# Kernel tuning notes

Hardware: AMD Instinct MI355X
Metric: run time of the kernel (lower is better)

The kernel has to match this reference:

```python
import jax, jax.numpy as jnp
import numpy as np

NUM_EXPERTS = 8
TOP_K = 2
N_TOKENS = 4096
HIDDEN = 1024
EXPERT_DIM = 4096


def setup_inputs() -> dict:
    key = jax.random.key(0)
    ks = jax.random.split(key, 4)
    x = jax.random.normal(ks[0], (N_TOKENS, HIDDEN), dtype=jnp.float32)
    Wg = jax.random.normal(ks[1], (HIDDEN, NUM_EXPERTS), dtype=jnp.float32) * 0.02
    bg = jnp.zeros((NUM_EXPERTS,), dtype=jnp.float32)
    W1 = jax.random.normal(ks[2], (NUM_EXPERTS, HIDDEN, EXPERT_DIM), dtype=jnp.float32) * 0.02
    b1 = jnp.zeros((NUM_EXPERTS, EXPERT_DIM), dtype=jnp.float32)
    W2 = jax.random.normal(ks[3], (NUM_EXPERTS, EXPERT_DIM, HIDDEN), dtype=jnp.float32) * 0.02
    b2 = jnp.zeros((NUM_EXPERTS, HIDDEN), dtype=jnp.float32)
    return {"x": x, "Wg": Wg, "bg": bg, "W1": W1, "b1": b1, "W2": W2, "b2": b2}


def reference(x, Wg, bg, W1, b1, W2, b2):
    # Gating: softmax over experts, then top-k routing with renormalized gates.
    gate_probs = jax.nn.softmax(x @ Wg + bg, axis=-1)          # [N, E]
    top_gates, top_idx = jax.lax.top_k(gate_probs, TOP_K)      # [N, K]
    top_gates = top_gates / jnp.sum(top_gates, axis=-1, keepdims=True)
    # Per-(token, expert) combine weight: sum of gates routed to that expert.
    combine = jnp.sum(
        jax.nn.one_hot(top_idx, NUM_EXPERTS, dtype=x.dtype) * top_gates[..., None],
        axis=1,
    )  # [N, E]
    # Expert MLPs: Linear -> ReLU -> Linear (dropout=0 at eval, norm=False).
    out = jnp.zeros_like(x)
    for e in range(NUM_EXPERTS):
        h = jax.nn.relu(x @ W1[e] + b1[e])                      # [N, expert_dim]
        y = h @ W2[e] + b2[e]                                   # [N, hidden]
        out = out + combine[:, e:e + 1] * y
    # Switch-style auxiliary load-balancing loss.
    expert_counts = jnp.sum(gate_probs, axis=0)                 # [E]
    expert_fractions = expert_counts / jnp.sum(expert_counts)
    gate_means = jnp.mean(gate_probs, axis=0)
    aux_loss = NUM_EXPERTS * jnp.sum(expert_fractions * gate_means)
    return out, aux_loss
```

## Files before the change

### kernel.cpp

```cpp
#include <hip/hip_runtime.h>


typedef unsigned short u16;
typedef __bf16 bf16x8 __attribute__((ext_vector_type(8)));
typedef float  f32x4  __attribute__((ext_vector_type(4)));

#define NTOK 4096
#define HID  1024
#define EDIM 4096
#define NEXP 8
#define MAXMT 40

__device__ __forceinline__ u16 f32_bf16(float f) {
  unsigned int u = __float_as_uint(f);
  u += 0x7FFFu + ((u >> 16) & 1u);
  return (u16)(u >> 16);
}

__global__ void gate_kernel(const float* __restrict__ x,
                            const float* __restrict__ Wg,
                            const float* __restrict__ bg,
                            float* __restrict__ combine,
                            float* __restrict__ counts,
                            int* __restrict__ icnt,
                            int* __restrict__ top2idx,
                            float* __restrict__ top2g) {
  __shared__ float lc[NEXP];
  int t = threadIdx.x;
  if (t < NEXP) lc[t] = 0.f;
  __syncthreads();
  int token = blockIdx.x * 4 + (t >> 6);
  int lane = t & 63;
  float s[NEXP] = {};
  const float* xr = x + (size_t)token * HID;
  for (int h = lane; h < HID; h += 64) {
    float xv = xr[h];
    const float* wrow = Wg + (size_t)h * NEXP;
#pragma unroll
    for (int e = 0; e < NEXP; ++e) s[e] += xv * wrow[e];
  }
#pragma unroll
  for (int off = 32; off > 0; off >>= 1) {
#pragma unroll
    for (int e = 0; e < NEXP; ++e) s[e] += __shfl_xor(s[e], off);
  }
  float m = -1e30f;
#pragma unroll
  for (int e = 0; e < NEXP; ++e) { s[e] += bg[e]; m = fmaxf(m, s[e]); }
  float p[NEXP]; float sum = 0.f;
#pragma unroll
  for (int e = 0; e < NEXP; ++e) { p[e] = expf(s[e] - m); sum += p[e]; }
  float inv = 1.f / sum;
#pragma unroll
  for (int e = 0; e < NEXP; ++e) p[e] *= inv;
  int i1 = 0; float g1 = p[0];
#pragma unroll
  for (int e = 1; e < NEXP; ++e) if (p[e] > g1) { g1 = p[e]; i1 = e; }
  int i2 = -1; float g2 = -1.f;
#pragma unroll
  for (int e = 0; e < NEXP; ++e) if (e != i1 && p[e] > g2) { g2 = p[e]; i2 = e; }
  float ginv = 1.f / (g1 + g2);
  if (lane == 0) {
#pragma unroll
    for (int e = 0; e < NEXP; ++e) {
      float c = (e == i1) ? g1 * ginv : (e == i2) ? g2 * ginv : 0.f;
      combine[(size_t)token * NEXP + e] = c;
      atomicAdd(&lc[e], p[e]);
    }
    top2idx[token * 2] = i1; top2idx[token * 2 + 1] = i2;
    top2g[token * 2] = g1 * ginv; top2g[token * 2 + 1] = g2 * ginv;
    atomicAdd(&icnt[i1], 1); atomicAdd(&icnt[i2], 1);
  }
  __syncthreads();
  if (t < NEXP) atomicAdd(&counts[t], lc[t]);
}

__global__ void aux_kernel(const float* __restrict__ counts, float* __restrict__ aux_out) {
  float s = 0.f;
#pragma unroll
  for (int e = 0; e < NEXP; ++e) s += counts[e];
  float a = 0.f;
#pragma unroll
  for (int e = 0; e < NEXP; ++e) a += (counts[e] / s) * (counts[e] / (float)NTOK);
  aux_out[0] = (float)NEXP * a;
}

__global__ void off_kernel(const int* __restrict__ icnt, int* __restrict__ ioff,
                           int* __restrict__ cursor, int* __restrict__ nmtP,
                           int* __restrict__ mtE, int* __restrict__ mtRow0,
                           int* __restrict__ mtValid) {
  int s = 0;
  int loc[NEXP];
  for (int e = 0; e < NEXP; ++e) { loc[e] = s; ioff[e] = s; s += icnt[e]; cursor[e] = 0; }
  int nm = 0;
  for (int e = 0; e < NEXP; ++e) {
    int c = icnt[e];
    int tiles = (c + 255) >> 8;
    for (int mt = 0; mt < tiles; ++mt) {
      mtE[nm] = e; mtRow0[nm] = loc[e] + (mt << 8);
      int v = c - (mt << 8); mtValid[nm] = v > 256 ? 256 : v;
      nm++;
    }
  }
  nmtP[0] = nm;
}

__global__ void fill_kernel(const int* __restrict__ top2idx, const int* __restrict__ ioff,
                            int* __restrict__ cursor, int* __restrict__ tok) {
  int i = blockIdx.x * 256 + threadIdx.x;
  if (i >= NTOK * 2) return;
  int t = i >> 1, k = i & 1;
  int e = top2idx[i];
  int pos = atomicAdd(&cursor[e], 1);
  tok[ioff[e] + pos] = t | (k << 16);
}

__global__ void cvt_kernel(const float* __restrict__ in, u16* __restrict__ out) {
  size_t i = ((size_t)blockIdx.x * 256 + threadIdx.x) * 4;
  float4 v = *(const float4*)(in + i);
  ushort4 o = make_ushort4(f32_bf16(v.x), f32_bf16(v.y), f32_bf16(v.z), f32_bf16(v.w));
  *(ushort4*)(out + i) = o;
}

__global__ __launch_bounds__(256) void cvtT_kernel(const float* __restrict__ W,
                                                   u16* __restrict__ WT, int R, int C) {
  __shared__ u16 tile[64][66];
  int t = threadIdx.x;
  size_t eoff = (size_t)blockIdx.z * R * C;
  int c0 = blockIdx.x * 64, r0 = blockIdx.y * 64;
  const float* Wp = W + eoff + (size_t)r0 * C + c0;
  u16* WTp = WT + eoff + (size_t)c0 * R + r0;
#pragma unroll
  for (int p = 0; p < 4; ++p) {
    int idx = p * 256 + t;
    int row = idx >> 4;
    int col = (idx & 15) * 4;
    float4 v = *(const float4*)(Wp + (size_t)row * C + col);
    tile[row][col + 0] = f32_bf16(v.x);
    tile[row][col + 1] = f32_bf16(v.y);
    tile[row][col + 2] = f32_bf16(v.z);
    tile[row][col + 3] = f32_bf16(v.w);
  }
  __syncthreads();
#pragma unroll
  for (int p = 0; p < 4; ++p) {
    int idx = p * 256 + t;
    int oc = idx >> 4;
    int orow = (idx & 15) * 4;
    ushort4 o;
    o.x = tile[orow + 0][oc];
    o.y = tile[orow + 1][oc];
    o.z = tile[orow + 2][oc];
    o.w = tile[orow + 3][oc];
    *(ushort4*)(WTp + (size_t)oc * R + orow) = o;
  }
}

template<int MODE, int SPLITK>
__global__ __launch_bounds__(256, 2) void gemm_sparse(
    const u16* __restrict__ A, const u16* __restrict__ Wt,
    const int* __restrict__ nmtP, const int* __restrict__ mtE,
    const int* __restrict__ mtRow0, const int* __restrict__ mtValid,
    const int* __restrict__ tok,
    const float* __restrict__ bias, u16* __restrict__ Hout,
    float* __restrict__ Y0, float* __restrict__ Y1)
{
  constexpr int KDIM = (MODE == 1) ? HID : EDIM;
  constexpr int NDIM = (MODE == 1) ? EDIM : HID;
  constexpr int NT = NDIM / 128;
  constexpr int NK = KDIM / 32 / SPLITK;

  const int nwg = gridDim.x;
  const int q = nwg >> 3, rr8 = nwg & 7;
  const int xcd = blockIdx.x & 7, jj = blockIdx.x >> 3;
  int item = (xcd < rr8 ? xcd * (q + 1) : rr8 * (q + 1) + (xcd - rr8) * q) + jj;

  if (item >= nmtP[0] * NT * SPLITK) return;
  const int gmt = item / (NT * SPLITK);
  const int sk  = (item / NT) % SPLITK;
  const int nt  = item % NT;
  const int e = mtE[gmt], row0 = mtRow0[gmt], valid = mtValid[gmt];
  const int kbeg = sk * (KDIM / SPLITK);

  __shared__ __align__(16) u16 As[3][256 * 32];
  __shared__ __align__(16) u16 Bs[3][128 * 32];
  const int t = threadIdx.x;
  const int lane = t & 63;
  const int w = t >> 6;
  const int wr = w >> 1, wc = w & 1;
  const int bn0 = nt << 7;
  const int kq = lane >> 4;
  const int r  = lane & 15;

  const u16* Bb = Wt + ((size_t)e * NDIM + bn0) * KDIM;

  size_t arow[4];
#pragma unroll
  for (int c = 0; c < 4; ++c) {
    int idx = c * 256 + t;
    int row = idx >> 2;
    if (MODE == 1) {
      int rw = (row < valid) ? row : 0;
      arow[c] = (size_t)(tok[row0 + rw] & 0xFFFF) * KDIM;
    } else {
      arow[c] = (size_t)(row0 + row) * KDIM;
    }
  }

  auto stage = [&](int buf, int k0) {
#pragma unroll
    for (int c = 0; c < 4; ++c) {
      int idx = c * 256 + t;
      int row = idx >> 2;
      int kc  = (((idx & 3) ^ ((row >> 1) & 3))) << 3;
      __builtin_amdgcn_global_load_lds(
          (const __attribute__((address_space(1))) void*)(A + arow[c] + k0 + kc),
          (__attribute__((address_space(3))) void*)(&As[buf][idx * 8]), 16, 0, 0);
    }
#pragma unroll
    for (int c = 0; c < 2; ++c) {
      int idx = c * 256 + t;
      int row = idx >> 2;
      int kc  = (((idx & 3) ^ ((row >> 1) & 3))) << 3;
      __builtin_amdgcn_global_load_lds(
          (const __attribute__((address_space(1))) void*)(Bb + (size_t)row * KDIM + k0 + kc),
          (__attribute__((address_space(3))) void*)(&Bs[buf][idx * 8]), 16, 0, 0);
    }
  };

  f32x4 acc[4][8] = {};

  stage(0, kbeg);
  stage(1, kbeg + 32);
  int cb = 0, sb = 2;
  for (int ks = 0; ks < NK; ++ks) {
    if (ks + 1 < NK) asm volatile("s_waitcnt vmcnt(6)" ::: "memory");
    else             asm volatile("s_waitcnt vmcnt(0)" ::: "memory");
    __builtin_amdgcn_s_barrier();
    __builtin_amdgcn_sched_barrier(0);
    if (ks + 2 < NK) stage(sb, kbeg + (ks + 2) * 32);

    bf16x8 af[8], bfr[4];
#pragma unroll
    for (int f = 0; f < 8; ++f) {
      int ra = wr * 128 + f * 16 + r;
      af[f]  = *(const bf16x8*)(&As[cb][ra * 32 + ((kq ^ ((ra >> 1) & 3)) << 3)]);
    }
#pragma unroll
    for (int f = 0; f < 4; ++f) {
      int rb = wc * 64 + f * 16 + r;
      bfr[f] = *(const bf16x8*)(&Bs[cb][rb * 32 + ((kq ^ ((rb >> 1) & 3)) << 3)]);
    }
    __builtin_amdgcn_s_setprio(1);
#pragma unroll
    for (int fm = 0; fm < 8; ++fm) {
#pragma unroll
      for (int fn = 0; fn < 4; ++fn) {
        acc[fn][fm] = __builtin_amdgcn_mfma_f32_16x16x32_bf16(bfr[fn], af[fm], acc[fn][fm], 0, 0, 0);
      }
    }
    __builtin_amdgcn_s_setprio(0);
    cb = (cb == 2) ? 0 : cb + 1;
    sb = (sb == 2) ? 0 : sb + 1;
  }

  if (MODE == 1) {
#pragma unroll
    for (int fm = 0; fm < 8; ++fm) {
      int lr = wr * 128 + fm * 16 + r;
      if (lr < valid) {
        u16* hrow = Hout + (size_t)(row0 + lr) * EDIM;
#pragma unroll
        for (int fn = 0; fn < 4; ++fn) {
          int col0 = bn0 + wc * 64 + fn * 16 + kq * 4;
          float4 bv = *(const float4*)(bias + (size_t)e * EDIM + col0);
          float v0 = acc[fn][fm][0] + bv.x; v0 = v0 > 0.f ? v0 : 0.f;
          float v1 = acc[fn][fm][1] + bv.y; v1 = v1 > 0.f ? v1 : 0.f;
          float v2 = acc[fn][fm][2] + bv.z; v2 = v2 > 0.f ? v2 : 0.f;
          float v3 = acc[fn][fm][3] + bv.w; v3 = v3 > 0.f ? v3 : 0.f;
          ushort4 h = make_ushort4(f32_bf16(v0), f32_bf16(v1), f32_bf16(v2), f32_bf16(v3));
          *(ushort4*)(hrow + col0) = h;
        }
      }
    }
  } else {
    float* Yb = (sk == 0) ? Y0 : Y1;
#pragma unroll
    for (int fm = 0; fm < 8; ++fm) {
      int lr = wr * 128 + fm * 16 + r;
      if (lr < valid) {
        int entry = tok[row0 + lr];
        int tt = entry & 0xFFFF, ss = entry >> 16;
        float* yrow = Yb + ((size_t)ss * NTOK + tt) * HID;
#pragma unroll
        for (int fn = 0; fn < 4; ++fn) {
          int col0 = bn0 + wc * 64 + fn * 16 + kq * 4;
          float4 o;
          if (sk == 0) {
            float4 bv = *(const float4*)(bias + (size_t)e * HID + col0);
            o.x = acc[fn][fm][0] + bv.x;
            o.y = acc[fn][fm][1] + bv.y;
            o.z = acc[fn][fm][2] + bv.z;
            o.w = acc[fn][fm][3] + bv.w;
          } else {
            o.x = acc[fn][fm][0];
            o.y = acc[fn][fm][1];
            o.z = acc[fn][fm][2];
            o.w = acc[fn][fm][3];
          }
          *(float4*)(yrow + col0) = o;
        }
      }
    }
  }
}

__global__ void final_kernel(const float* __restrict__ top2g,
                             const float* __restrict__ Ys0,
                             const float* __restrict__ Ys1,
                             float* __restrict__ out) {
  size_t idx4 = (size_t)blockIdx.x * 256 + threadIdx.x;
  size_t base = idx4 * 4;
  int t = (int)(base >> 10);
  float g0 = top2g[t * 2], g1 = top2g[t * 2 + 1];
  float4 a0 = *(const float4*)(Ys0 + base);
  float4 b0 = *(const float4*)(Ys1 + base);
  float4 a1 = *(const float4*)(Ys0 + (size_t)NTOK * HID + base);
  float4 b1 = *(const float4*)(Ys1 + (size_t)NTOK * HID + base);
  float4 o;
  o.x = g0 * (a0.x + b0.x) + g1 * (a1.x + b1.x);
  o.y = g0 * (a0.y + b0.y) + g1 * (a1.y + b1.y);
  o.z = g0 * (a0.z + b0.z) + g1 * (a1.z + b1.z);
  o.w = g0 * (a0.w + b0.w) + g1 * (a1.w + b1.w);
  *(float4*)(out + base) = o;
}

__global__ void init_out_kernel(const float* __restrict__ combine,
                                const float* __restrict__ b2,
                                float* __restrict__ out) {
  size_t idx = (size_t)blockIdx.x * 256 + threadIdx.x;
  int i = (int)(idx >> 10), j = (int)(idx & 1023);
  float v = 0.f;
#pragma unroll
  for (int e = 0; e < NEXP; ++e) v += combine[(size_t)i * NEXP + e] * b2[e * HID + j];
  out[idx] = v;
}

template<int MODE>
__global__ __launch_bounds__(256) void gemm_kernel(
    const u16* __restrict__ A, const u16* __restrict__ BT,
    int M, int N, int K,
    const float* __restrict__ bias, u16* __restrict__ Hout,
    const float* __restrict__ combine, int expert, float* __restrict__ Out)
{
  __shared__ __align__(16) u16 As[128 * 32];
  __shared__ __align__(16) u16 Bs[128 * 32];
  const int t = threadIdx.x;
  const int lane = t & 63;
  const int w = t >> 6;
  const int wr = w >> 1, wc = w & 1;
  const int nbn = N >> 7;
  const int bm0 = (int)(blockIdx.x / nbn) << 7;
  const int bn0 = (int)(blockIdx.x % nbn) << 7;
  const int kq = lane >> 4;
  const int r  = lane & 15;
  f32x4 acc[4][4] = {};
  const u16* Ab = A + (size_t)bm0 * K;
  const u16* Bb = BT + (size_t)bn0 * K;
  for (int k0 = 0; k0 < K; k0 += 32) {
    __syncthreads();
#pragma unroll
    for (int c = 0; c < 2; ++c) {
      int idx = c * 256 + t;
      int row = idx >> 2;
      int kc  = (idx & 3) << 3;
      __builtin_amdgcn_global_load_lds(
          (const __attribute__((address_space(1))) void*)(Ab + (size_t)row * K + k0 + kc),
          (__attribute__((address_space(3))) void*)(As + idx * 8), 16, 0, 0);
      __builtin_amdgcn_global_load_lds(
          (const __attribute__((address_space(1))) void*)(Bb + (size_t)row * K + k0 + kc),
          (__attribute__((address_space(3))) void*)(Bs + idx * 8), 16, 0, 0);
    }
    __syncthreads();
    bf16x8 af[4], bfr[4];
#pragma unroll
    for (int f = 0; f < 4; ++f) {
      af[f]  = *(const bf16x8*)(As + (wr * 64 + f * 16 + r) * 32 + kq * 8);
      bfr[f] = *(const bf16x8*)(Bs + (wc * 64 + f * 16 + r) * 32 + kq * 8);
    }
#pragma unroll
    for (int fm = 0; fm < 4; ++fm) {
#pragma unroll
      for (int fn = 0; fn < 4; ++fn) {
        acc[fm][fn] = __builtin_amdgcn_mfma_f32_16x16x32_bf16(af[fm], bfr[fn], acc[fm][fn], 0, 0, 0);
      }
    }
  }
  if (MODE == 1) {
#pragma unroll
    for (int fn = 0; fn < 4; ++fn) {
      int col = bn0 + wc * 64 + fn * 16 + r;
      float bv = bias[col];
#pragma unroll
      for (int fm = 0; fm < 4; ++fm) {
#pragma unroll
        for (int j = 0; j < 4; ++j) {
          int row = bm0 + wr * 64 + fm * 16 + kq * 4 + j;
          float v = acc[fm][fn][j] + bv;
          v = v > 0.f ? v : 0.f;
          Hout[(size_t)row * N + col] = f32_bf16(v);
        }
      }
    }
  } else {
#pragma unroll
    for (int fm = 0; fm < 4; ++fm) {
      float cg[4];
#pragma unroll
      for (int j = 0; j < 4; ++j) {
        int row = bm0 + wr * 64 + fm * 16 + kq * 4 + j;
        cg[j] = combine[(size_t)row * NEXP + expert];
      }
#pragma unroll
      for (int fn = 0; fn < 4; ++fn) {
        int col = bn0 + wc * 64 + fn * 16 + r;
#pragma unroll
        for (int j = 0; j < 4; ++j) {
          int row = bm0 + wr * 64 + fm * 16 + kq * 4 + j;
          Out[(size_t)row * N + col] += cg[j] * acc[fm][fn][j];
        }
      }
    }
  }
}

extern "C" void kernel_launch(void* const* d_in, const int* in_sizes, int n_in,
                              void* d_out, int out_size, void* d_ws, size_t ws_size,
                              hipStream_t stream) {
  (void)in_sizes; (void)n_in; (void)out_size;
  const float* x  = (const float*)d_in[0];
  const float* Wg = (const float*)d_in[1];
  const float* bg = (const float*)d_in[2];
  const float* W1 = (const float*)d_in[3];
  const float* b1 = (const float*)d_in[4];
  const float* W2 = (const float*)d_in[5];
  const float* b2 = (const float*)d_in[6];
  float* out = (float*)d_out;

  char* ws = (char*)d_ws;
  float* counts  = (float*)(ws);
  int*   icnt    = (int*)(ws + 64);
  int*   ioff    = (int*)(ws + 128);
  int*   cursor  = (int*)(ws + 192);
  int*   nmtP    = (int*)(ws + 256);
  int*   mtE     = (int*)(ws + 512);
  int*   mtRow0  = (int*)(ws + 1024);
  int*   mtValid = (int*)(ws + 1536);
  int*   top2idx = (int*)(ws + 4096);
  float* top2g   = (float*)(ws + 36864);
  int*   tok     = (int*)(ws + 69632);
  float* combine = (float*)(ws + 131072);

  const size_t MB = 1024 * 1024;
  u16* xbf = (u16*)(ws + 1 * MB);

  const size_t REQ = 241 * MB;
  bool sparse = ws_size >= REQ;

  hipMemsetAsync(ws, 0, 1024, stream);
  gate_kernel<<<NTOK / 4, 256, 0, stream>>>(x, Wg, bg, combine, counts, icnt, top2idx, top2g);
  aux_kernel<<<1, 1, 0, stream>>>(counts, out + (size_t)NTOK * HID);
  cvt_kernel<<<(NTOK * HID) / 1024, 256, 0, stream>>>(x, xbf);

  if (sparse) {
    u16* w1tA    = (u16*)(ws + 9 * MB);
    u16* w2tA    = (u16*)(ws + 73 * MB);
    u16* H       = (u16*)(ws + 137 * MB);
    float* Ys0   = (float*)(ws + 209 * MB);
    float* Ys1   = (float*)(ws + 9 * MB);

    cvtT_kernel<<<dim3(EDIM / 64, HID / 64, NEXP), 256, 0, stream>>>(W1, w1tA, HID, EDIM);
    cvtT_kernel<<<dim3(HID / 64, EDIM / 64, NEXP), 256, 0, stream>>>(W2, w2tA, EDIM, HID);
    off_kernel<<<1, 1, 0, stream>>>(icnt, ioff, cursor, nmtP, mtE, mtRow0, mtValid);
    fill_kernel<<<(NTOK * 2 + 255) / 256, 256, 0, stream>>>(top2idx, ioff, cursor, tok);

    gemm_sparse<1, 1><<<MAXMT * (EDIM / 128), 256, 0, stream>>>(
        xbf, w1tA, nmtP, mtE, mtRow0, mtValid, tok, b1, H, nullptr, nullptr);
    gemm_sparse<2, 2><<<MAXMT * (HID / 128) * 2, 256, 0, stream>>>(
        H, w2tA, nmtP, mtE, mtRow0, mtValid, tok, b2, nullptr, Ys0, Ys1);
    final_kernel<<<(NTOK * HID / 4) / 256, 256, 0, stream>>>(top2g, Ys0, Ys1, out);
  } else {
    u16* w1t = (u16*)(ws + 9 * MB);
    u16* w2t = (u16*)(ws + 17 * MB);
    u16* H   = (u16*)(ws + 25 * MB);
    init_out_kernel<<<(NTOK * HID) / 256, 256, 0, stream>>>(combine, b2, out);
    for (int e = 0; e < NEXP; ++e) {
      cvtT_kernel<<<dim3(EDIM / 64, HID / 64, 1), 256, 0, stream>>>(
          W1 + (size_t)e * HID * EDIM, w1t, HID, EDIM);
      gemm_kernel<1><<<(NTOK / 128) * (EDIM / 128), 256, 0, stream>>>(
          xbf, w1t, NTOK, EDIM, HID, b1 + (size_t)e * EDIM, H, nullptr, 0, nullptr);
      cvtT_kernel<<<dim3(HID / 64, EDIM / 64, 1), 256, 0, stream>>>(
          W2 + (size_t)e * EDIM * HID, w2t, EDIM, HID);
      gemm_kernel<2><<<(NTOK / 128) * (HID / 128), 256, 0, stream>>>(
          H, w2t, NTOK, HID, EDIM, nullptr, nullptr, combine, e, out);
    }
  }
}
```

Baseline: 514.5 us.

## Restructure sparse expert GEMM into 8-wave 64-deep tiles with interleaved staging

The sparse expert GEMM moves from 4 to 8 waves per workgroup and from a K-step of 32 to 64. The three-buffer LDS ring becomes a double buffer, with a wider XOR swizzle. The first GEMM's N tile doubles to 256, so each A tile is reused across more output columns. Loads for the next K tile are split into pieces issued between four compute phases, overlapping global-to-LDS traffic with MFMA work. The larger tiles use more LDS per workgroup (about 128KB for the first GEMM), which cuts occupancy, and the added barriers may cost throughput.

```diff
diff --git a/kernel.cpp b/kernel.cpp
--- a/kernel.cpp
+++ b/kernel.cpp
@@ -157,7 +157,7 @@
 }
 
 template<int MODE, int SPLITK>
-__global__ __launch_bounds__(256, 2) void gemm_sparse(
+__global__ __launch_bounds__(512, 2) void gemm_sparse(
     const u16* __restrict__ A, const u16* __restrict__ Wt,
     const int* __restrict__ nmtP, const int* __restrict__ mtE,
     const int* __restrict__ mtRow0, const int* __restrict__ mtValid,
@@ -167,8 +167,11 @@
 {
   constexpr int KDIM = (MODE == 1) ? HID : EDIM;
   constexpr int NDIM = (MODE == 1) ? EDIM : HID;
-  constexpr int NT = NDIM / 128;
-  constexpr int NK = KDIM / 32 / SPLITK;
+  constexpr int BN   = (MODE == 1) ? 256 : 128;
+  constexpr int NT   = NDIM / BN;
+  constexpr int FN   = BN / 64;
+  constexpr int NKT  = KDIM / 64 / SPLITK;
+  constexpr int BH   = BN / 128;
 
   const int nwg = gridDim.x;
   const int q = nwg >> 3, rr8 = nwg & 7;
@@ -181,24 +184,26 @@
   const int nt  = item % NT;
   const int e = mtE[gmt], row0 = mtRow0[gmt], valid = mtValid[gmt];
   const int kbeg = sk * (KDIM / SPLITK);
-
-  __shared__ __align__(16) u16 As[3][256 * 32];
-  __shared__ __align__(16) u16 Bs[3][128 * 32];
+  const int bn0 = nt * BN;
+
+  __shared__ __align__(16) u16 As[2][256 * 64];
+  __shared__ __align__(16) u16 Bs[2][BN * 64];
+
   const int t = threadIdx.x;
   const int lane = t & 63;
   const int w = t >> 6;
-  const int wr = w >> 1, wc = w & 1;
-  const int bn0 = nt << 7;
+  const int wr = w >> 2, wc = w & 3;
   const int kq = lane >> 4;
   const int r  = lane & 15;
+  const int srow = t >> 3;
+  const int schunk = t & 7;
 
   const u16* Bb = Wt + ((size_t)e * NDIM + bn0) * KDIM;
 
   size_t arow[4];
 #pragma unroll
   for (int c = 0; c < 4; ++c) {
-    int idx = c * 256 + t;
-    int row = idx >> 2;
+    int row = c * 64 + srow;
     if (MODE == 1) {
       int rw = (row < valid) ? row : 0;
       arow[c] = (size_t)(tok[row0 + rw] & 0xFFFF) * KDIM;
@@ -207,61 +212,79 @@
     }
   }
 
-  auto stage = [&](int buf, int k0) {
-#pragma unroll
-    for (int c = 0; c < 4; ++c) {
-      int idx = c * 256 + t;
-      int row = idx >> 2;
-      int kc  = (((idx & 3) ^ ((row >> 1) & 3))) << 3;
+  auto stageA = [&](int buf, int kt, int h) {
+#pragma unroll
+    for (int l = 0; l < 2; ++l) {
+      int row = h * 128 + l * 64 + srow;
+      int kc  = (schunk ^ (row & 7)) << 3;
       __builtin_amdgcn_global_load_lds(
-          (const __attribute__((address_space(1))) void*)(A + arow[c] + k0 + kc),
-          (__attribute__((address_space(3))) void*)(&As[buf][idx * 8]), 16, 0, 0);
-    }
-#pragma unroll
-    for (int c = 0; c < 2; ++c) {
-      int idx = c * 256 + t;
-      int row = idx >> 2;
-      int kc  = (((idx & 3) ^ ((row >> 1) & 3))) << 3;
+          (const __attribute__((address_space(1))) void*)(A + arow[h * 2 + l] + kbeg + kt * 64 + kc),
+          (__attribute__((address_space(3))) void*)(&As[buf][row * 64 + schunk * 8]), 16, 0, 0);
+    }
+  };
+  auto stageB = [&](int buf, int kt, int h) {
+#pragma unroll
+    for (int l = 0; l < 2; ++l) {
+      int row = h * 128 + l * 64 + srow;
+      int kc  = (schunk ^ (row & 7)) << 3;
       __builtin_amdgcn_global_load_lds(
-          (const __attribute__((address_space(1))) void*)(Bb + (size_t)row * KDIM + k0 + kc),
-          (__attribute__((address_space(3))) void*)(&Bs[buf][idx * 8]), 16, 0, 0);
+          (const __attribute__((address_space(1))) void*)(Bb + (size_t)row * KDIM + kbeg + kt * 64 + kc),
+          (__attribute__((address_space(3))) void*)(&Bs[buf][row * 64 + schunk * 8]), 16, 0, 0);
     }
   };
 
-  f32x4 acc[4][8] = {};
-
-  stage(0, kbeg);
-  stage(1, kbeg + 32);
-  int cb = 0, sb = 2;
-  for (int ks = 0; ks < NK; ++ks) {
-    if (ks + 1 < NK) asm volatile("s_waitcnt vmcnt(6)" ::: "memory");
-    else             asm volatile("s_waitcnt vmcnt(0)" ::: "memory");
+  f32x4 acc[FN][8] = {};
+  bf16x8 bfr[FN];
+
+  auto phase = [&](int cur, int ks, int fmh) {
+    bf16x8 af[4];
+    if (fmh == 0) {
+#pragma unroll
+      for (int j = 0; j < FN; ++j) {
+        int rb = wc * (BN / 4) + j * 16 + r;
+        bfr[j] = *(const bf16x8*)(&Bs[cur][rb * 64 + (((ks * 4 + kq) ^ (rb & 7)) << 3)]);
+      }
+    }
+#pragma unroll
+    for (int f = 0; f < 4; ++f) {
+      int ra = wr * 128 + (fmh * 4 + f) * 16 + r;
+      af[f] = *(const bf16x8*)(&As[cur][ra * 64 + (((ks * 4 + kq) ^ (ra & 7)) << 3)]);
+    }
+    asm volatile("s_waitcnt lgkmcnt(0)" ::: "memory");
+    __builtin_amdgcn_sched_barrier(0);
+    __builtin_amdgcn_s_setprio(1);
+#pragma unroll
+    for (int f = 0; f < 4; ++f) {
+#pragma unroll
+      for (int j = 0; j < FN; ++j) {
+        acc[j][fmh * 4 + f] =
+            __builtin_amdgcn_mfma_f32_16x16x32_bf16(bfr[j], af[f], acc[j][fmh * 4 + f], 0, 0, 0);
+      }
+    }
+    __builtin_amdgcn_s_setprio(0);
+    __builtin_amdgcn_s_barrier();
+  };
+
+  stageA(0, 0, 0); stageA(0, 0, 1);
+  stageB(0, 0, 0); if (BH == 2) stageB(0, 0, 1);
+
+  int cur = 0;
+  for (int kt = 0; kt < NKT; ++kt) {
+    const bool more = (kt + 1 < NKT);
+    if (more) stageA(cur ^ 1, kt + 1, 0);
+    if (more) asm volatile("s_waitcnt vmcnt(2)" ::: "memory");
+    else      asm volatile("s_waitcnt vmcnt(0)" ::: "memory");
     __builtin_amdgcn_s_barrier();
     __builtin_amdgcn_sched_barrier(0);
-    if (ks + 2 < NK) stage(sb, kbeg + (ks + 2) * 32);
-
-    bf16x8 af[8], bfr[4];
-#pragma unroll
-    for (int f = 0; f < 8; ++f) {
-      int ra = wr * 128 + f * 16 + r;
-      af[f]  = *(const bf16x8*)(&As[cb][ra * 32 + ((kq ^ ((ra >> 1) & 3)) << 3)]);
-    }
-#pragma unroll
-    for (int f = 0; f < 4; ++f) {
-      int rb = wc * 64 + f * 16 + r;
-      bfr[f] = *(const bf16x8*)(&Bs[cb][rb * 32 + ((kq ^ ((rb >> 1) & 3)) << 3)]);
-    }
-    __builtin_amdgcn_s_setprio(1);
-#pragma unroll
-    for (int fm = 0; fm < 8; ++fm) {
-#pragma unroll
-      for (int fn = 0; fn < 4; ++fn) {
-        acc[fn][fm] = __builtin_amdgcn_mfma_f32_16x16x32_bf16(bfr[fn], af[fm], acc[fn][fm], 0, 0, 0);
-      }
-    }
-    __builtin_amdgcn_s_setprio(0);
-    cb = (cb == 2) ? 0 : cb + 1;
-    sb = (sb == 2) ? 0 : sb + 1;
+
+    phase(cur, 0, 0);
+    if (more) stageA(cur ^ 1, kt + 1, 1);
+    phase(cur, 0, 1);
+    if (more) stageB(cur ^ 1, kt + 1, 0);
+    phase(cur, 1, 0);
+    if (more && BH == 2) stageB(cur ^ 1, kt + 1, 1);
+    phase(cur, 1, 1);
+    cur ^= 1;
   }
 
   if (MODE == 1) {
@@ -271,8 +294,8 @@
       if (lr < valid) {
         u16* hrow = Hout + (size_t)(row0 + lr) * EDIM;
 #pragma unroll
-        for (int fn = 0; fn < 4; ++fn) {
-          int col0 = bn0 + wc * 64 + fn * 16 + kq * 4;
+        for (int fn = 0; fn < FN; ++fn) {
+          int col0 = bn0 + wc * (BN / 4) + fn * 16 + kq * 4;
           float4 bv = *(const float4*)(bias + (size_t)e * EDIM + col0);
           float v0 = acc[fn][fm][0] + bv.x; v0 = v0 > 0.f ? v0 : 0.f;
           float v1 = acc[fn][fm][1] + bv.y; v1 = v1 > 0.f ? v1 : 0.f;
@@ -293,8 +316,8 @@
         int tt = entry & 0xFFFF, ss = entry >> 16;
         float* yrow = Yb + ((size_t)ss * NTOK + tt) * HID;
 #pragma unroll
-        for (int fn = 0; fn < 4; ++fn) {
-          int col0 = bn0 + wc * 64 + fn * 16 + kq * 4;
+        for (int fn = 0; fn < FN; ++fn) {
+          int col0 = bn0 + wc * (BN / 4) + fn * 16 + kq * 4;
           float4 o;
           if (sk == 0) {
             float4 bv = *(const float4*)(bias + (size_t)e * HID + col0);
@@ -484,9 +507,9 @@
     off_kernel<<<1, 1, 0, stream>>>(icnt, ioff, cursor, nmtP, mtE, mtRow0, mtValid);
     fill_kernel<<<(NTOK * 2 + 255) / 256, 256, 0, stream>>>(top2idx, ioff, cursor, tok);
 
-    gemm_sparse<1, 1><<<MAXMT * (EDIM / 128), 256, 0, stream>>>(
+    gemm_sparse<1, 1><<<MAXMT * (EDIM / 256), 512, 0, stream>>>(
         xbf, w1tA, nmtP, mtE, mtRow0, mtValid, tok, b1, H, nullptr, nullptr);
-    gemm_sparse<2, 2><<<MAXMT * (HID / 128) * 2, 256, 0, stream>>>(
+    gemm_sparse<2, 2><<<MAXMT * (HID / 128) * 2, 512, 0, stream>>>(
         H, w2tA, nmtP, mtE, mtRow0, mtValid, tok, b2, nullptr, Ys0, Ys1);
     final_kernel<<<(NTOK * HID / 4) / 256, 256, 0, stream>>>(top2g, Ys0, Ys1, out);
   } else {
```

New measurement: 619.2 us. 20.3% more time.

## Switch GEMM to double-buffered LDS with three blocks per CU and M-major tile order

Applied to the files above, without the earlier changes.

Cuts the LDS ring from three stages to two and raises launch bounds from 2 to 3 blocks per CU, aiming for more resident workgroups to hide latency. Work items are also reordered so consecutive items walk across M-tiles for the same N-tile and split, which changes weight-tile reuse in cache. In exchange the prefetch distance drops to one stage with a full vmcnt(0) wait each iteration, and the tighter register budget under 3 waves may cause spills with the 128-float accumulator.

```diff
diff --git a/kernel.cpp b/kernel.cpp
--- a/kernel.cpp
+++ b/kernel.cpp
@@ -157,7 +157,7 @@
 }
 
 template<int MODE, int SPLITK>
-__global__ __launch_bounds__(256, 2) void gemm_sparse(
+__global__ __launch_bounds__(256, 3) void gemm_sparse(
     const u16* __restrict__ A, const u16* __restrict__ Wt,
     const int* __restrict__ nmtP, const int* __restrict__ mtE,
     const int* __restrict__ mtRow0, const int* __restrict__ mtValid,
@@ -175,20 +175,22 @@
   const int xcd = blockIdx.x & 7, jj = blockIdx.x >> 3;
   int item = (xcd < rr8 ? xcd * (q + 1) : rr8 * (q + 1) + (xcd - rr8) * q) + jj;
 
-  if (item >= nmtP[0] * NT * SPLITK) return;
-  const int gmt = item / (NT * SPLITK);
-  const int sk  = (item / NT) % SPLITK;
-  const int nt  = item % NT;
+  const int nmt = nmtP[0];
+  if (item >= nmt * NT * SPLITK) return;
+  const int idx2 = item / nmt;
+  const int gmt  = item - idx2 * nmt;
+  const int nt   = idx2 / SPLITK;
+  const int sk   = idx2 - nt * SPLITK;
   const int e = mtE[gmt], row0 = mtRow0[gmt], valid = mtValid[gmt];
   const int kbeg = sk * (KDIM / SPLITK);
-
-  __shared__ __align__(16) u16 As[3][256 * 32];
-  __shared__ __align__(16) u16 Bs[3][128 * 32];
+  const int bn0 = nt << 7;
+
+  __shared__ __align__(16) u16 As[2][256 * 32];
+  __shared__ __align__(16) u16 Bs[2][128 * 32];
   const int t = threadIdx.x;
   const int lane = t & 63;
   const int w = t >> 6;
   const int wr = w >> 1, wc = w & 1;
-  const int bn0 = nt << 7;
   const int kq = lane >> 4;
   const int r  = lane & 15;
 
@@ -197,8 +199,7 @@
   size_t arow[4];
 #pragma unroll
   for (int c = 0; c < 4; ++c) {
-    int idx = c * 256 + t;
-    int row = idx >> 2;
+    int row = (c * 256 + t) >> 2;
     if (MODE == 1) {
       int rw = (row < valid) ? row : 0;
       arow[c] = (size_t)(tok[row0 + rw] & 0xFFFF) * KDIM;
@@ -231,26 +232,26 @@
   f32x4 acc[4][8] = {};
 
   stage(0, kbeg);
-  stage(1, kbeg + 32);
-  int cb = 0, sb = 2;
+  int cur = 0;
   for (int ks = 0; ks < NK; ++ks) {
-    if (ks + 1 < NK) asm volatile("s_waitcnt vmcnt(6)" ::: "memory");
-    else             asm volatile("s_waitcnt vmcnt(0)" ::: "memory");
+    asm volatile("s_waitcnt vmcnt(0)" ::: "memory");
     __builtin_amdgcn_s_barrier();
     __builtin_amdgcn_sched_barrier(0);
-    if (ks + 2 < NK) stage(sb, kbeg + (ks + 2) * 32);
+    if (ks + 1 < NK) stage(cur ^ 1, kbeg + (ks + 1) * 32);
 
     bf16x8 af[8], bfr[4];
 #pragma unroll
     for (int f = 0; f < 8; ++f) {
       int ra = wr * 128 + f * 16 + r;
-      af[f]  = *(const bf16x8*)(&As[cb][ra * 32 + ((kq ^ ((ra >> 1) & 3)) << 3)]);
+      af[f]  = *(const bf16x8*)(&As[cur][ra * 32 + ((kq ^ ((ra >> 1) & 3)) << 3)]);
     }
 #pragma unroll
     for (int f = 0; f < 4; ++f) {
       int rb = wc * 64 + f * 16 + r;
-      bfr[f] = *(const bf16x8*)(&Bs[cb][rb * 32 + ((kq ^ ((rb >> 1) & 3)) << 3)]);
-    }
+      bfr[f] = *(const bf16x8*)(&Bs[cur][rb * 32 + ((kq ^ ((rb >> 1) & 3)) << 3)]);
+    }
+    asm volatile("s_waitcnt lgkmcnt(0)" ::: "memory");
+    __builtin_amdgcn_sched_barrier(0);
     __builtin_amdgcn_s_setprio(1);
 #pragma unroll
     for (int fm = 0; fm < 8; ++fm) {
@@ -260,8 +261,7 @@
       }
     }
     __builtin_amdgcn_s_setprio(0);
-    cb = (cb == 2) ? 0 : cb + 1;
-    sb = (sb == 2) ? 0 : sb + 1;
+    cur ^= 1;
   }
 
   if (MODE == 1) {
```

Measured after the change: 932.2 us. 81.2% more time.
